# Optimization experiments

Hardware: AMD Instinct MI355X
Metric: run time of the kernel (lower is better)

Reference implementation:

```python
import jax, jax.numpy as jnp
import numpy as np
import math

B, T, D, N = 4, 2048, 1024, 16
HD = D // N
SCALE = math.sqrt(D)  # source scales by sqrt(d_key) = sqrt(full model dim)
BIG = 1e9

def setup_inputs() -> dict:
    key = jax.random.key(0)
    ks = jax.random.split(key, 11)
    s = 1.0 / math.sqrt(D)
    return {
        "query": jax.random.normal(ks[0], (B, T, D), jnp.float32),
        "key": jax.random.normal(ks[1], (B, T, D), jnp.float32),
        "value": jax.random.normal(ks[2], (B, T, D), jnp.float32),
        "wq_w": jax.random.normal(ks[3], (D, D), jnp.float32) * s,
        "wq_b": jnp.zeros((D,), jnp.float32),
        "wk_w": jax.random.normal(ks[4], (D, D), jnp.float32) * s,
        "wk_b": jnp.zeros((D,), jnp.float32),
        "wv_w": jax.random.normal(ks[5], (D, D), jnp.float32) * s,
        "wv_b": jnp.zeros((D,), jnp.float32),
        "wo_w": jax.random.normal(ks[6], (D, D), jnp.float32) * s,
        "wo_b": jnp.zeros((D,), jnp.float32),
    }

def reference(query, key, value, wq_w, wq_b, wk_w, wk_b, wv_w, wv_b, wo_w, wo_b):
    # projections (torch Linear equiv; weights stored as (in,out))
    q = query @ wq_w + wq_b
    k = key @ wk_w + wk_b
    v = value @ wv_w + wv_b
    # split heads: (B,T,D) -> (B,N,T,HD)
    def split(x):
        return x.reshape(B, T, N, HD).transpose(0, 2, 1, 3)
    q, k, v = split(q), split(k), split(v)
    # dot products (source does elementwise mul+sum == einsum)
    scores = jnp.einsum('bnqd,bnkd->bnqk', q, k)
    # only_attend_front: subtract 1e9 on strict upper triangle
    tri = jnp.triu(jnp.ones((T, T), scores.dtype), 1) * BIG
    scores = scores - tri
    logits = scores / SCALE
    probs = jax.nn.softmax(logits, axis=-1)
    # zero rows where every position is masked (source trick)
    alive = ((scores <= -BIG / 2).sum(-1, keepdims=True) < T).astype(probs.dtype)
    probs = probs * alive
    out = jnp.einsum('bnqk,bnkd->bnqd', probs, v)  # (B,N,T,HD)
    out = out.transpose(0, 2, 1, 3).reshape(B, T, D)
    return out @ wo_w + wo_b
```

## Files before the change

### kernel.cpp

```cpp
#include <hip/hip_runtime.h>
#include <hip/hip_bf16.h>

#define BB 4
#define TT 2048
#define DD 1024
#define NHEAD 16
#define HDIM 64
#define NKT 16

typedef __bf16 v8bf __attribute__((ext_vector_type(8)));
typedef __bf16 v4bf __attribute__((ext_vector_type(4)));
typedef float  v4f  __attribute__((ext_vector_type(4)));

#define C2SCALE 0.04508422376f

__device__ __forceinline__ void gl2lds16(const void* g, void* l) {
  __builtin_amdgcn_global_load_lds(
      (__attribute__((address_space(1))) const void*)g,
      (__attribute__((address_space(3))) void*)l, 16, 0, 0);
}

__global__ __launch_bounds__(256) void prep(
    const float* __restrict__ qsrc, const float* __restrict__ ksrc,
    const float* __restrict__ vsrc,
    const float* __restrict__ w0, const float* __restrict__ w1,
    const float* __restrict__ w2, const float* __restrict__ w3,
    __bf16* __restrict__ qdst, __bf16* __restrict__ kdst,
    __bf16* __restrict__ vdst,
    __bf16* __restrict__ t0, __bf16* __restrict__ t1,
    __bf16* __restrict__ t2, __bf16* __restrict__ t3) {
  constexpr int STR = 72;
  __shared__ __bf16 sh[64 * STR];
  int bx = blockIdx.x, tid = threadIdx.x;
  if (bx < 12288) {
    const float* src = bx < 4096 ? qsrc : bx < 8192 ? ksrc : vsrc;
    __bf16* dst = bx < 4096 ? qdst : bx < 8192 ? kdst : vdst;
    int i = (bx & 4095) * 256 + tid;
    const float4* s = (const float4*)src + (size_t)i * 2;
    float4 f0 = s[0], f1 = s[1];
    v8bf v;
    v[0] = (__bf16)f0.x; v[1] = (__bf16)f0.y; v[2] = (__bf16)f0.z; v[3] = (__bf16)f0.w;
    v[4] = (__bf16)f1.x; v[5] = (__bf16)f1.y; v[6] = (__bf16)f1.z; v[7] = (__bf16)f1.w;
    *(v8bf*)(dst + (size_t)i * 8) = v;
  } else {
    int idx = bx - 12288;
    int z = idx >> 8;
    const float* W = z == 0 ? w0 : z == 1 ? w1 : z == 2 ? w2 : w3;
    __bf16* Wt = z == 0 ? t0 : z == 1 ? t1 : z == 2 ? t2 : t3;
    int n0 = (idx & 15) * 64, k0 = ((idx >> 4) & 15) * 64;
#pragma unroll
    for (int p = 0; p < 4; ++p) {
      int c = tid + p * 256;
      int r = c >> 4, off = (c & 15) * 4;
      float4 f = *(const float4*)(W + (size_t)(k0 + r) * DD + n0 + off);
      __bf16* d = &sh[r * STR + off];
      d[0] = (__bf16)f.x; d[1] = (__bf16)f.y; d[2] = (__bf16)f.z; d[3] = (__bf16)f.w;
    }
    __syncthreads();
#pragma unroll
    for (int p = 0; p < 2; ++p) {
      int c = tid + p * 256;
      int nr = c >> 3, koff = (c & 7) * 8;
      v8bf v;
#pragma unroll
      for (int j = 0; j < 8; ++j) v[j] = sh[(koff + j) * STR + nr];
      *(v8bf*)(Wt + (size_t)(n0 + nr) * DD + k0 + koff) = v;
    }
  }
}

__global__ __launch_bounds__(512, 2) void gemm8p(
    const __bf16* __restrict__ A0p, const __bf16* __restrict__ A1p,
    const __bf16* __restrict__ A2p,
    const __bf16* __restrict__ W0p, const __bf16* __restrict__ W1p,
    const __bf16* __restrict__ W2p,
    const float* __restrict__ b0p, const float* __restrict__ b1p,
    const float* __restrict__ b2p,
    __bf16* __restrict__ Qp, __bf16* __restrict__ Kp,
    __bf16* __restrict__ VTb, float* __restrict__ Cf, int mode) {
  extern __shared__ __bf16 lds[];
  int tid = threadIdx.x, wave = tid >> 6, lane = tid & 63;
  int quad = lane >> 4, l15 = lane & 15, swz = l15 & 7;
  int wm2 = wave >> 2, wn4 = wave & 3;
  int lin = blockIdx.x;
  int qx = gridDim.x >> 3;
  int wg = (lin >> 3) + (lin & 7) * qx;
  int z = wg >> 7, t = wg & 127;
  int m0 = (t >> 2) * 256, n0 = (t & 3) * 256;
  const __bf16* __restrict__ A  = z == 0 ? A0p : z == 1 ? A1p : A2p;
  const __bf16* __restrict__ Wt = z == 0 ? W0p : z == 1 ? W1p : W2p;
  const float* __restrict__ bias = z == 0 ? b0p : z == 1 ? b1p : b2p;

  v4f acc[8][4];
#pragma unroll
  for (int mi = 0; mi < 8; ++mi)
#pragma unroll
    for (int ni = 0; ni < 4; ++ni) acc[mi][ni] = (v4f){0.f, 0.f, 0.f, 0.f};

#define STAGE(XP, x0, base, h, kt) do {                                     \
  int k0s = (kt) * 64;                                                      \
_Pragma("unroll")                                                           \
  for (int w = 0; w < 2; ++w) {                                             \
    int idx = w * 512 + tid;                                                \
    int srow = (h) * 128 + (idx >> 3);                                      \
    int g = (idx & 7) ^ (srow & 7);                                         \
    gl2lds16((XP) + (size_t)((x0) + srow) * DD + k0s + g * 8,               \
             lds + (base) + (h) * 8192 + idx * 8);                          \
  }                                                                         \
} while (0)

#define LD_A(d, mh) do {                                                    \
_Pragma("unroll")                                                           \
  for (int ks = 0; ks < 2; ++ks)                                            \
_Pragma("unroll")                                                           \
    for (int jm = 0; jm < 4; ++jm)                                          \
      afr[ks][jm] = *(const v8bf*)&lds[(d) * 32768 +                        \
          (wm2 * 64 + (mh) * 128 + jm * 16 + l15) * 64 +                    \
          ((ks * 4 + quad) ^ swz) * 8];                                     \
} while (0)

#define LD_B(d, nh) do {                                                    \
_Pragma("unroll")                                                           \
  for (int ks = 0; ks < 2; ++ks)                                            \
_Pragma("unroll")                                                           \
    for (int jn = 0; jn < 2; ++jn)                                          \
      bfr[nh][ks][jn] = *(const v8bf*)&lds[(d) * 32768 + 16384 +            \
          (wn4 * 32 + (nh) * 128 + jn * 16 + l15) * 64 +                    \
          ((ks * 4 + quad) ^ swz) * 8];                                     \
} while (0)

#define SYNC_MID(VM) do {                                                   \
  asm volatile("s_waitcnt vmcnt(" #VM ")" ::: "memory");                    \
  __builtin_amdgcn_s_barrier();                                             \
  asm volatile("s_waitcnt lgkmcnt(0)" ::: "memory");                        \
} while (0)

#define MFMA16(mh, nh) do {                                                 \
  __builtin_amdgcn_s_setprio(1);                                            \
_Pragma("unroll")                                                           \
  for (int ks = 0; ks < 2; ++ks)                                            \
_Pragma("unroll")                                                           \
    for (int jm = 0; jm < 4; ++jm)                                          \
_Pragma("unroll")                                                           \
      for (int jn = 0; jn < 2; ++jn)                                        \
        acc[(mh) * 4 + jm][(nh) * 2 + jn] =                                 \
            __builtin_amdgcn_mfma_f32_16x16x32_bf16(                        \
                afr[ks][jm], bfr[nh][ks][jn],                               \
                acc[(mh) * 4 + jm][(nh) * 2 + jn], 0, 0, 0);                \
  __builtin_amdgcn_s_setprio(0);                                            \
  __builtin_amdgcn_s_barrier();                                             \
} while (0)

#define TILE(d, jt) do {                                                    \
  v8bf afr[2][4]; v8bf bfr[2][2][2];                                        \
                                                  \
  LD_A(d, 0); LD_B(d, 0);                                                   \
  if ((jt) + 1 < NKT) STAGE(A, m0, ((d) ^ 1) * 32768, 1, (jt) + 1);         \
  SYNC_MID(6); MFMA16(0, 0);                                                \
                                                        \
  LD_B(d, 1);                                                               \
  if ((jt) + 1 < NKT) STAGE(Wt, n0, ((d) ^ 1) * 32768 + 16384, 1, (jt) + 1);\
  SYNC_MID(6); MFMA16(0, 1);                                                \
                                                        \
  LD_A(d, 1);                                                               \
  if ((jt) + 2 < NKT) STAGE(A, m0, (d) * 32768, 0, (jt) + 2);               \
  SYNC_MID(6); MFMA16(1, 0);                                                \
                                                        \
  if ((jt) + 2 < NKT) STAGE(Wt, n0, (d) * 32768 + 16384, 0, (jt) + 2);      \
  SYNC_MID(6); MFMA16(1, 1);                                                \
} while (0)

  STAGE(A, m0, 0, 0, 0);
  STAGE(Wt, n0, 16384, 0, 0);
  STAGE(A, m0, 0, 1, 0);
  STAGE(Wt, n0, 16384, 1, 0);
  STAGE(A, m0, 32768, 0, 1);
  STAGE(Wt, n0, 32768 + 16384, 0, 1);
  asm volatile("s_waitcnt vmcnt(8)" ::: "memory");
  __builtin_amdgcn_s_barrier();

  for (int j2 = 0; j2 < 7; ++j2) {
    TILE(0, j2 * 2);
    TILE(1, j2 * 2 + 1);
  }
  TILE(0, 14);
  asm volatile("s_waitcnt vmcnt(0)" ::: "memory");
  __builtin_amdgcn_s_barrier();
  TILE(1, 15);

#pragma unroll
  for (int ni = 0; ni < 4; ++ni) {
    int col = n0 + wn4 * 32 + (ni >> 1) * 128 + (ni & 1) * 16 + l15;
    float bv = bias[col];
    if (mode) {
#pragma unroll
      for (int mi = 0; mi < 8; ++mi) {
        int row = m0 + wm2 * 64 + (mi >> 2) * 128 + (mi & 3) * 16 + quad * 4;
#pragma unroll
        for (int r = 0; r < 4; ++r)
          Cf[(size_t)(row + r) * DD + col] = acc[mi][ni][r] + bv;
      }
    } else if (z == 2) {
      int b = m0 >> 11;
      __bf16* rowp = VTb + ((size_t)(b * 16 + (col >> 6)) * 64 + (col & 63)) * TT;
      int tb0 = (m0 & 2047) + wm2 * 64;
#pragma unroll
      for (int mi = 0; mi < 8; ++mi) {
        int tb = tb0 + (mi >> 2) * 128 + (mi & 3) * 16 + quad * 4;
        v4bf o;
#pragma unroll
        for (int r = 0; r < 4; ++r) o[r] = (__bf16)(acc[mi][ni][r] + bv);
        *(v4bf*)(rowp + tb) = o;
      }
    } else {
      __bf16* C = z == 0 ? Qp : Kp;
      float scale = z == 0 ? C2SCALE : 1.0f;
#pragma unroll
      for (int mi = 0; mi < 8; ++mi) {
        int row = m0 + wm2 * 64 + (mi >> 2) * 128 + (mi & 3) * 16 + quad * 4;
#pragma unroll
        for (int r = 0; r < 4; ++r)
          C[(size_t)(row + r) * DD + col] = (__bf16)((acc[mi][ni][r] + bv) * scale);
      }
    }
  }
#undef TILE
#undef MFMA16
#undef SYNC_MID
#undef LD_B
#undef LD_A
#undef STAGE
}

__global__ __launch_bounds__(256) void attn_bal(const __bf16* __restrict__ Q,
                                                const __bf16* __restrict__ K,
                                                const __bf16* __restrict__ VT,
                                                __bf16* __restrict__ O) {
  __shared__ __bf16 ksh[2][64 * 64];
  __shared__ __bf16 vsh[2][64 * 64];
  __shared__ __bf16 psh[128 * 64];
  int tid = threadIdx.x, wave = tid >> 6, lane = tid & 63;
  int quad = lane >> 4, l15 = lane & 15;
  int swz = l15 & 7;
  int lin = blockIdx.x + 8 * blockIdx.y;
  int c = lin & 7, t = lin >> 3;
  int xq = t & 7;
  int bh = c + ((t >> 3) << 3);
  int b = bh >> 4, h = bh & 15;
  const __bf16* Qb = Q + (size_t)(b * TT) * DD + h * HDIM;
  const __bf16* Kb = K + (size_t)(b * TT) * DD + h * HDIM;
  const __bf16* Vb = VT + (size_t)bh * HDIM * TT;
  __bf16* Ob = O + (size_t)(b * TT) * DD + h * HDIM;

  v8bf ones;
#pragma unroll
  for (int j = 0; j < 8; ++j) ones[j] = (__bf16)1.0f;

  for (int phase = 0; phase < 2; ++phase) {
    int qi = phase ? 15 - xq : xq;
    int q0 = qi * 128;
    int ktiles = 2 * qi + 2;

#pragma unroll
    for (int i = 0; i < 4; ++i) {
      int cc = wave * 256 + i * 64 + lane;
      int row = cc >> 3, g = (cc & 7) ^ (row & 7);
      gl2lds16(Qb + (size_t)(q0 + row) * DD + g * 8, psh + wave * 2048 + i * 512);
    }
#pragma unroll
    for (int i = 0; i < 2; ++i) {
      int cc = wave * 128 + i * 64 + lane;
      int row = cc >> 3, g = (cc & 7) ^ (row & 7);
      gl2lds16(Kb + (size_t)row * DD + g * 8, &ksh[0][wave * 1024 + i * 512]);
      gl2lds16(Vb + (size_t)row * TT + g * 8, &vsh[0][wave * 1024 + i * 512]);
    }
    __builtin_amdgcn_s_waitcnt(0);
    __syncthreads();

    v8bf qf[2][2];
#pragma unroll
    for (int set = 0; set < 2; ++set)
#pragma unroll
      for (int ks = 0; ks < 2; ++ks)
        qf[set][ks] = *(v8bf*)&psh[(wave * 32 + set * 16 + l15) * 64 + ((ks * 4 + quad) ^ swz) * 8];

    int qg[2] = {q0 + wave * 32 + l15, q0 + wave * 32 + 16 + l15};
    v4f oacc[2][4], lracc[2];
#pragma unroll
    for (int set = 0; set < 2; ++set) {
      lracc[set] = (v4f){0.f, 0.f, 0.f, 0.f};
#pragma unroll
      for (int jm = 0; jm < 4; ++jm) oacc[set][jm] = (v4f){0.f, 0.f, 0.f, 0.f};
    }

    int pbuf = 0;
    for (int kt = 0; kt < ktiles; ++kt) {
      if (kt + 1 < ktiles) {
        int k0n = (kt + 1) * 64;
#pragma unroll
        for (int i = 0; i < 2; ++i) {
          int cc = wave * 128 + i * 64 + lane;
          int row = cc >> 3, g = (cc & 7) ^ (row & 7);
          gl2lds16(Kb + (size_t)(k0n + row) * DD + g * 8, &ksh[pbuf ^ 1][wave * 1024 + i * 512]);
          gl2lds16(Vb + (size_t)row * TT + k0n + g * 8, &vsh[pbuf ^ 1][wave * 1024 + i * 512]);
        }
      }
      int k0 = kt * 64;
      const __bf16* kshp = &ksh[pbuf][0];
      const __bf16* vshp = &vsh[pbuf][0];

      v4f s[2][4];
#pragma unroll
      for (int set = 0; set < 2; ++set)
#pragma unroll
        for (int jf = 0; jf < 4; ++jf) s[set][jf] = (v4f){0.f, 0.f, 0.f, 0.f};
#pragma unroll
      for (int ks = 0; ks < 2; ++ks) {
        int sw = ((ks * 4 + quad) ^ swz) * 8;
#pragma unroll
        for (int jf = 0; jf < 4; ++jf) {
          v8bf kf = *(v8bf*)&kshp[(jf * 16 + l15) * 64 + sw];
          s[0][jf] = __builtin_amdgcn_mfma_f32_16x16x32_bf16(kf, qf[0][ks], s[0][jf], 0, 0, 0);
          s[1][jf] = __builtin_amdgcn_mfma_f32_16x16x32_bf16(kf, qf[1][ks], s[1][jf], 0, 0, 0);
        }
      }

      bool diag = (kt >= 2 * qi);
#pragma unroll
      for (int set = 0; set < 2; ++set) {
        int qrow = wave * 32 + set * 16 + l15;
        __bf16* prow = &psh[qrow * 64];
#pragma unroll
        for (int jf = 0; jf < 4; ++jf) {
          v4bf pk;
#pragma unroll
          for (int r = 0; r < 4; ++r) {
            float p = __builtin_amdgcn_exp2f(s[set][jf][r]);
            if (diag) {
              int kg = k0 + jf * 16 + quad * 4 + r;
              if (kg > qg[set]) p = 0.f;
            }
            pk[r] = (__bf16)p;
          }
          int chunk = jf * 2 + (quad >> 1);
          *(v4bf*)&prow[(chunk ^ swz) * 8 + (quad & 1) * 4] = pk;
        }
      }

#pragma unroll
      for (int ks = 0; ks < 2; ++ks) {
        int sw = ((ks * 4 + quad) ^ swz) * 8;
        v8bf pb0 = *(v8bf*)&psh[(wave * 32 + l15) * 64 + sw];
        v8bf pb1 = *(v8bf*)&psh[(wave * 32 + 16 + l15) * 64 + sw];
        lracc[0] = __builtin_amdgcn_mfma_f32_16x16x32_bf16(ones, pb0, lracc[0], 0, 0, 0);
        lracc[1] = __builtin_amdgcn_mfma_f32_16x16x32_bf16(ones, pb1, lracc[1], 0, 0, 0);
#pragma unroll
        for (int jm = 0; jm < 4; ++jm) {
          v8bf vf = *(v8bf*)&vshp[(jm * 16 + l15) * 64 + sw];
          oacc[0][jm] = __builtin_amdgcn_mfma_f32_16x16x32_bf16(vf, pb0, oacc[0][jm], 0, 0, 0);
          oacc[1][jm] = __builtin_amdgcn_mfma_f32_16x16x32_bf16(vf, pb1, oacc[1][jm], 0, 0, 0);
        }
      }

      __builtin_amdgcn_s_waitcnt(0);
      __syncthreads();
      pbuf ^= 1;
    }

#pragma unroll
    for (int set = 0; set < 2; ++set) {
      float inv = 1.0f / lracc[set][0];
      int q = q0 + wave * 32 + set * 16 + l15;
#pragma unroll
      for (int jm = 0; jm < 4; ++jm) {
        v4bf o;
#pragma unroll
        for (int r = 0; r < 4; ++r) o[r] = (__bf16)(oacc[set][jm][r] * inv);
        *(v4bf*)(Ob + (size_t)q * DD + jm * 16 + quad * 4) = o;
      }
    }
  }
}

extern "C" void kernel_launch(void* const* d_in, const int* in_sizes, int n_in,
                              void* d_out, int out_size, void* d_ws, size_t ws_size,
                              hipStream_t stream) {
  const float* query = (const float*)d_in[0];
  const float* key_  = (const float*)d_in[1];
  const float* value = (const float*)d_in[2];
  const float* wq_w = (const float*)d_in[3];
  const float* wq_b = (const float*)d_in[4];
  const float* wk_w = (const float*)d_in[5];
  const float* wk_b = (const float*)d_in[6];
  const float* wv_w = (const float*)d_in[7];
  const float* wv_b = (const float*)d_in[8];
  const float* wo_w = (const float*)d_in[9];
  const float* wo_b = (const float*)d_in[10];

  char* ws = (char*)d_ws;
  const size_t MB = (size_t)1 << 20;
  __bf16* wqT = (__bf16*)(ws + 0 * MB);
  __bf16* wkT = (__bf16*)(ws + 2 * MB);
  __bf16* wvT = (__bf16*)(ws + 4 * MB);
  __bf16* woT = (__bf16*)(ws + 6 * MB);
  __bf16* Qc  = (__bf16*)(ws + 8 * MB);
  __bf16* Kc  = (__bf16*)(ws + 24 * MB);
  __bf16* Vc  = (__bf16*)(ws + 40 * MB);
  __bf16* Qp  = (__bf16*)(ws + 56 * MB);
  __bf16* Kp  = (__bf16*)(ws + 72 * MB);
  __bf16* VTb = (__bf16*)(ws + 88 * MB);
  __bf16* Ab  = (__bf16*)(ws + 8 * MB);
  float* out = (float*)d_out;

  static int attr_done = 0;
  if (!attr_done) {
    hipFuncSetAttribute((const void*)gemm8p,
                        hipFuncAttributeMaxDynamicSharedMemorySize, 131072);
    attr_done = 1;
  }

  dim3 tb(256);
  prep<<<dim3(13312), tb, 0, stream>>>(query, key_, value, wq_w, wk_w, wv_w, wo_w,
                                       Qc, Kc, Vc, wqT, wkT, wvT, woT);
  gemm8p<<<dim3(384), dim3(512), 131072, stream>>>(
      Qc, Kc, Vc, wqT, wkT, wvT, wq_b, wk_b, wv_b, Qp, Kp, VTb, nullptr, 0);
  attn_bal<<<dim3(8, 64), tb, 0, stream>>>(Qp, Kp, VTb, Ab);
  gemm8p<<<dim3(128), dim3(512), 131072, stream>>>(
      Ab, Ab, Ab, woT, woT, woT, wo_b, wo_b, wo_b, nullptr, nullptr, nullptr,
      out, 1);
}
```

Measured before the change: 349.8 us.

## Add dedicated 128x128 output GEMM, coarsen prep casts, retune GEMM waits, add MFMA priority

The output projection moves from the 256x256 gemm8p tile (128 blocks) to a new simpler 128x128-tile kernel with 512 blocks, so more CUs are busy. The prep cast kernel now has each block convert eight chunks, cutting the grid from 13312 to 2560 blocks. The QKV GEMM pipeline waits on vmcnt only once per tile instead of at every phase, and the attention kernel raises wave priority around its MFMA sections. Risks: the new out GEMM has no double buffering and stalls on a barrier every k-step, and the relaxed vmcnt waits could expose load latency or cause LDS hazards if the counts are wrong.

Result: faster. 337.0 us (-3.7%).

```diff
diff --git a/kernel.cpp b/kernel.cpp
--- a/kernel.cpp
+++ b/kernel.cpp
@@ -32,18 +32,22 @@
   constexpr int STR = 72;
   __shared__ __bf16 sh[64 * STR];
   int bx = blockIdx.x, tid = threadIdx.x;
-  if (bx < 12288) {
-    const float* src = bx < 4096 ? qsrc : bx < 8192 ? ksrc : vsrc;
-    __bf16* dst = bx < 4096 ? qdst : bx < 8192 ? kdst : vdst;
-    int i = (bx & 4095) * 256 + tid;
-    const float4* s = (const float4*)src + (size_t)i * 2;
-    float4 f0 = s[0], f1 = s[1];
-    v8bf v;
-    v[0] = (__bf16)f0.x; v[1] = (__bf16)f0.y; v[2] = (__bf16)f0.z; v[3] = (__bf16)f0.w;
-    v[4] = (__bf16)f1.x; v[5] = (__bf16)f1.y; v[6] = (__bf16)f1.z; v[7] = (__bf16)f1.w;
-    *(v8bf*)(dst + (size_t)i * 8) = v;
+  if (bx < 1536) {
+    int z = bx >> 9, ib = bx & 511;
+    const float* src = z == 0 ? qsrc : z == 1 ? ksrc : vsrc;
+    __bf16* dst = z == 0 ? qdst : z == 1 ? kdst : vdst;
+#pragma unroll
+    for (int k = 0; k < 8; ++k) {
+      int u = ib * 2048 + k * 256 + tid;
+      const float4* s = (const float4*)src + (size_t)u * 2;
+      float4 f0 = s[0], f1 = s[1];
+      v8bf v;
+      v[0] = (__bf16)f0.x; v[1] = (__bf16)f0.y; v[2] = (__bf16)f0.z; v[3] = (__bf16)f0.w;
+      v[4] = (__bf16)f1.x; v[5] = (__bf16)f1.y; v[6] = (__bf16)f1.z; v[7] = (__bf16)f1.w;
+      *(v8bf*)(dst + (size_t)u * 8) = v;
+    }
   } else {
-    int idx = bx - 12288;
+    int idx = bx - 1536;
     int z = idx >> 8;
     const float* W = z == 0 ? w0 : z == 1 ? w1 : z == 2 ? w2 : w3;
     __bf16* Wt = z == 0 ? t0 : z == 1 ? t1 : z == 2 ? t2 : t3;
@@ -77,7 +81,7 @@
     const float* __restrict__ b0p, const float* __restrict__ b1p,
     const float* __restrict__ b2p,
     __bf16* __restrict__ Qp, __bf16* __restrict__ Kp,
-    __bf16* __restrict__ VTb, float* __restrict__ Cf, int mode) {
+    __bf16* __restrict__ VTb) {
   extern __shared__ __bf16 lds[];
   int tid = threadIdx.x, wave = tid >> 6, lane = tid & 63;
   int quad = lane >> 4, l15 = lane & 15, swz = l15 & 7;
@@ -129,7 +133,12 @@
           ((ks * 4 + quad) ^ swz) * 8];                                     \
 } while (0)
 
-#define SYNC_MID(VM) do {                                                   \
+#define SYNC_PH() do {                                                      \
+  __builtin_amdgcn_s_barrier();                                             \
+  asm volatile("s_waitcnt lgkmcnt(0)" ::: "memory");                        \
+} while (0)
+
+#define SYNC_P4(VM) do {                                                    \
   asm volatile("s_waitcnt vmcnt(" #VM ")" ::: "memory");                    \
   __builtin_amdgcn_s_barrier();                                             \
   asm volatile("s_waitcnt lgkmcnt(0)" ::: "memory");                        \
@@ -151,23 +160,23 @@
   __builtin_amdgcn_s_barrier();                                             \
 } while (0)
 
-#define TILE(d, jt) do {                                                    \
+#define TILE(d, jt, VM4) do {                                               \
   v8bf afr[2][4]; v8bf bfr[2][2][2];                                        \
                                                   \
   LD_A(d, 0); LD_B(d, 0);                                                   \
   if ((jt) + 1 < NKT) STAGE(A, m0, ((d) ^ 1) * 32768, 1, (jt) + 1);         \
-  SYNC_MID(6); MFMA16(0, 0);                                                \
+  SYNC_PH(); MFMA16(0, 0);                                                  \
                                                         \
   LD_B(d, 1);                                                               \
   if ((jt) + 1 < NKT) STAGE(Wt, n0, ((d) ^ 1) * 32768 + 16384, 1, (jt) + 1);\
-  SYNC_MID(6); MFMA16(0, 1);                                                \
+  SYNC_PH(); MFMA16(0, 1);                                                  \
                                                         \
   LD_A(d, 1);                                                               \
   if ((jt) + 2 < NKT) STAGE(A, m0, (d) * 32768, 0, (jt) + 2);               \
-  SYNC_MID(6); MFMA16(1, 0);                                                \
-                                                        \
+  SYNC_PH(); MFMA16(1, 0);                                                  \
+                   \
   if ((jt) + 2 < NKT) STAGE(Wt, n0, (d) * 32768 + 16384, 0, (jt) + 2);      \
-  SYNC_MID(6); MFMA16(1, 1);                                                \
+  SYNC_P4(VM4); MFMA16(1, 1);                                               \
 } while (0)
 
   STAGE(A, m0, 0, 0, 0);
@@ -176,31 +185,21 @@
   STAGE(Wt, n0, 16384, 1, 0);
   STAGE(A, m0, 32768, 0, 1);
   STAGE(Wt, n0, 32768 + 16384, 0, 1);
-  asm volatile("s_waitcnt vmcnt(8)" ::: "memory");
+  asm volatile("s_waitcnt vmcnt(4)" ::: "memory");
   __builtin_amdgcn_s_barrier();
 
   for (int j2 = 0; j2 < 7; ++j2) {
-    TILE(0, j2 * 2);
-    TILE(1, j2 * 2 + 1);
-  }
-  TILE(0, 14);
-  asm volatile("s_waitcnt vmcnt(0)" ::: "memory");
-  __builtin_amdgcn_s_barrier();
-  TILE(1, 15);
+    TILE(0, j2 * 2, 4);
+    TILE(1, j2 * 2 + 1, 4);
+  }
+  TILE(0, 14, 0);
+  TILE(1, 15, 0);
 
 #pragma unroll
   for (int ni = 0; ni < 4; ++ni) {
     int col = n0 + wn4 * 32 + (ni >> 1) * 128 + (ni & 1) * 16 + l15;
     float bv = bias[col];
-    if (mode) {
-#pragma unroll
-      for (int mi = 0; mi < 8; ++mi) {
-        int row = m0 + wm2 * 64 + (mi >> 2) * 128 + (mi & 3) * 16 + quad * 4;
-#pragma unroll
-        for (int r = 0; r < 4; ++r)
-          Cf[(size_t)(row + r) * DD + col] = acc[mi][ni][r] + bv;
-      }
-    } else if (z == 2) {
+    if (z == 2) {
       int b = m0 >> 11;
       __bf16* rowp = VTb + ((size_t)(b * 16 + (col >> 6)) * 64 + (col & 63)) * TT;
       int tb0 = (m0 & 2047) + wm2 * 64;
@@ -226,10 +225,86 @@
   }
 #undef TILE
 #undef MFMA16
-#undef SYNC_MID
+#undef SYNC_P4
+#undef SYNC_PH
 #undef LD_B
 #undef LD_A
 #undef STAGE
+}
+
+__device__ __forceinline__ void gemm_core(const __bf16* __restrict__ A,
+                                          const __bf16* __restrict__ Wt,
+                                          int m0, int n0,
+                                          __bf16* ash, __bf16* bsh,
+                                          int wave, int lane, int quad, int l15,
+                                          v4f acc[4][4]) {
+  int wm = (wave & 1) * 64, wn = (wave >> 1) * 64;
+  for (int k0 = 0; k0 < DD; k0 += 64) {
+    __syncthreads();
+#pragma unroll
+    for (int i = 0; i < 4; ++i) {
+      int c = wave * 256 + i * 64 + lane;
+      int row = c >> 3, g = (c & 7) ^ (row & 7);
+      gl2lds16(A + (size_t)(m0 + row) * DD + k0 + g * 8, ash + wave * 2048 + i * 512);
+      gl2lds16(Wt + (size_t)(n0 + row) * DD + k0 + g * 8, bsh + wave * 2048 + i * 512);
+    }
+    __syncthreads();
+#pragma unroll
+    for (int ks = 0; ks < 2; ++ks) {
+      int sw = (((ks * 4 + quad) ^ (l15 & 7))) * 8;
+      v8bf a[4], b[4];
+#pragma unroll
+      for (int jm = 0; jm < 4; ++jm) a[jm] = *(v8bf*)&ash[(wm + jm * 16 + l15) * 64 + sw];
+#pragma unroll
+      for (int jn = 0; jn < 4; ++jn) b[jn] = *(v8bf*)&bsh[(wn + jn * 16 + l15) * 64 + sw];
+#pragma unroll
+      for (int jm = 0; jm < 4; ++jm)
+#pragma unroll
+        for (int jn = 0; jn < 4; ++jn)
+          acc[jm][jn] = __builtin_amdgcn_mfma_f32_16x16x32_bf16(a[jm], b[jn], acc[jm][jn], 0, 0, 0);
+    }
+  }
+}
+
+__device__ __forceinline__ void swz_tiles(int& m0, int& n0) {
+  int lin = blockIdx.x + 8 * blockIdx.y;
+  int c = lin & 7, t = lin >> 3;
+  n0 = (t & 7) * 128;
+  m0 = (c + ((t >> 3) << 3)) * 128;
+}
+
+__global__ __launch_bounds__(256) void gemm_out(const __bf16* __restrict__ A,
+                                                const __bf16* __restrict__ Wt,
+                                                const float* __restrict__ bias,
+                                                float* __restrict__ C) {
+  __shared__ __bf16 ash[128 * 64];
+  __shared__ __bf16 bsh[128 * 64];
+  int tid = threadIdx.x, wave = tid >> 6, lane = tid & 63;
+  int quad = lane >> 4, l15 = lane & 15;
+  int m0, n0;
+  swz_tiles(m0, n0);
+  int wm = (wave & 1) * 64, wn = (wave >> 1) * 64;
+  v4f acc[4][4];
+#pragma unroll
+  for (int jm = 0; jm < 4; ++jm)
+#pragma unroll
+    for (int jn = 0; jn < 4; ++jn) acc[jm][jn] = (v4f){0.f, 0.f, 0.f, 0.f};
+
+  gemm_core(A, Wt, m0, n0, ash, bsh, wave, lane, quad, l15, acc);
+
+#pragma unroll
+  for (int jn = 0; jn < 4; ++jn) {
+    int col = n0 + wn + jn * 16 + l15;
+    float bv = bias[col];
+#pragma unroll
+    for (int jm = 0; jm < 4; ++jm) {
+#pragma unroll
+      for (int r = 0; r < 4; ++r) {
+        int row = m0 + wm + jm * 16 + quad * 4 + r;
+        C[(size_t)row * DD + col] = acc[jm][jn][r] + bv;
+      }
+    }
+  }
 }
 
 __global__ __launch_bounds__(256) void attn_bal(const __bf16* __restrict__ Q,
@@ -314,6 +389,7 @@
       for (int set = 0; set < 2; ++set)
 #pragma unroll
         for (int jf = 0; jf < 4; ++jf) s[set][jf] = (v4f){0.f, 0.f, 0.f, 0.f};
+      __builtin_amdgcn_s_setprio(1);
 #pragma unroll
       for (int ks = 0; ks < 2; ++ks) {
         int sw = ((ks * 4 + quad) ^ swz) * 8;
@@ -324,6 +400,7 @@
           s[1][jf] = __builtin_amdgcn_mfma_f32_16x16x32_bf16(kf, qf[1][ks], s[1][jf], 0, 0, 0);
         }
       }
+      __builtin_amdgcn_s_setprio(0);
 
       bool diag = (kt >= 2 * qi);
 #pragma unroll
@@ -347,6 +424,7 @@
         }
       }
 
+      __builtin_amdgcn_s_setprio(1);
 #pragma unroll
       for (int ks = 0; ks < 2; ++ks) {
         int sw = ((ks * 4 + quad) ^ swz) * 8;
@@ -361,6 +439,7 @@
           oacc[1][jm] = __builtin_amdgcn_mfma_f32_16x16x32_bf16(vf, pb1, oacc[1][jm], 0, 0, 0);
         }
       }
+      __builtin_amdgcn_s_setprio(0);
 
       __builtin_amdgcn_s_waitcnt(0);
       __syncthreads();
@@ -420,12 +499,10 @@
   }
 
   dim3 tb(256);
-  prep<<<dim3(13312), tb, 0, stream>>>(query, key_, value, wq_w, wk_w, wv_w, wo_w,
-                                       Qc, Kc, Vc, wqT, wkT, wvT, woT);
+  prep<<<dim3(2560), tb, 0, stream>>>(query, key_, value, wq_w, wk_w, wv_w, wo_w,
+                                      Qc, Kc, Vc, wqT, wkT, wvT, woT);
   gemm8p<<<dim3(384), dim3(512), 131072, stream>>>(
-      Qc, Kc, Vc, wqT, wkT, wvT, wq_b, wk_b, wv_b, Qp, Kp, VTb, nullptr, 0);
+      Qc, Kc, Vc, wqT, wkT, wvT, wq_b, wk_b, wv_b, Qp, Kp, VTb);
   attn_bal<<<dim3(8, 64), tb, 0, stream>>>(Qp, Kp, VTb, Ab);
-  gemm8p<<<dim3(128), dim3(512), 131072, stream>>>(
-      Ab, Ab, Ab, woT, woT, woT, wo_b, wo_b, wo_b, nullptr, nullptr, nullptr,
-      out, 1);
-}
+  gemm_out<<<dim3(8, 64), tb, 0, stream>>>(Ab, woT, wo_b, out);
+}
```
